# Optimization experiments

Measured on AMD Instinct MI355X. Metric: run time of the kernel, lower is better.

Reference implementation:

```python
import jax, jax.numpy as jnp
import numpy as np

NBATCH, NUP, NDOWN, NMO, NCONF = 8192, 8, 8, 32, 64


def setup_inputs() -> dict:
    key = jax.random.key(0)
    k1, k2, k3, k4 = jax.random.split(key, 4)
    MO = jax.random.normal(k1, (NBATCH, NUP + NDOWN, NMO), dtype=jnp.float32)
    d2MO = jax.random.normal(k2, (NBATCH, NUP + NDOWN, NMO), dtype=jnp.float32)
    # each config = 8 distinct MO column indices per spin (distinct -> invertible A)
    configs_up = jnp.argsort(jax.random.uniform(k3, (NCONF, NMO)), axis=1)[:, :NUP].astype(jnp.int32)
    configs_down = jnp.argsort(jax.random.uniform(k4, (NCONF, NMO)), axis=1)[:, :NDOWN].astype(jnp.int32)
    return {"MO": MO, "d2MO": d2MO, "configs_up": configs_up, "configs_down": configs_down}


def _gather(M, elec_idx, cols):
    # M: (B, nelec, nmo) -> select electron rows then per-config MO columns
    Ms = M[:, elec_idx, :]                  # (B, n, nmo)
    A = jnp.take(Ms, cols, axis=2)          # (B, n, C, n)
    return jnp.transpose(A, (0, 2, 1, 3))   # (B, C, n, n)


def reference(MO, d2MO, configs_up, configs_down):
    nup = configs_up.shape[1]
    ndown = configs_down.shape[1]
    iup = jnp.arange(nup)
    idown = jnp.arange(nup, nup + ndown)

    Aup = _gather(MO, iup, configs_up)       # (B, C, nup, nup)
    Adn = _gather(MO, idown, configs_down)   # (B, C, ndown, ndown)
    d2up = _gather(d2MO, iup, configs_up)
    d2dn = _gather(d2MO, idown, configs_down)

    iAup = jnp.linalg.inv(Aup)
    iAdn = jnp.linalg.inv(Adn)

    # btrace(iA @ d2A) = sum_ij iA[i,j] * d2A[j,i]
    tr = lambda X, Y: jnp.einsum('bcij,bcji->bc', X, Y)
    out = tr(iAup, d2up) + tr(iAdn, d2dn)    # (B, C)

    # return_local_energy=False branch: multiply by product of determinants
    pd = jnp.linalg.det(Aup) * jnp.linalg.det(Adn)
    return -0.5 * out * pd
```

## Files before the change

### kernel.cpp

```cpp
#include <hip/hip_runtime.h>

#define NBATCH 8192
#define NELEC  16
#define NMO    32
#define NCONF  64
#define NS     8
#define TSTR   20
#define TSZ    (NMO * TSTR)

__device__ __forceinline__ void solve8T(const float* __restrict__ MOT,
                                        const float* __restrict__ D2T,
                                        const int (&cols)[NS], int eoff,
                                        float& det_out, float& tr_out)
{
    float A[NS][NS], D[NS][NS];
    #pragma unroll
    for (int j = 0; j < NS; ++j) {
        const float4* pa = (const float4*)(MOT + cols[j] * TSTR + eoff);
        const float4* pd = (const float4*)(D2T + cols[j] * TSTR + eoff);
        float4 a0 = pa[0], a1 = pa[1];
        float4 d0 = pd[0], d1 = pd[1];
        A[j][0] = a0.x; A[j][1] = a0.y; A[j][2] = a0.z; A[j][3] = a0.w;
        A[j][4] = a1.x; A[j][5] = a1.y; A[j][6] = a1.z; A[j][7] = a1.w;
        D[j][0] = d0.x; D[j][1] = d0.y; D[j][2] = d0.z; D[j][3] = d0.w;
        D[j][4] = d1.x; D[j][5] = d1.y; D[j][6] = d1.z; D[j][7] = d1.w;
    }

    float det = 1.0f;
    #pragma unroll
    for (int k = 0; k < NS; ++k) {
        det *= A[k][k];
        float pinv = __builtin_amdgcn_rcpf(A[k][k]);
        A[k][k] = pinv;
        #pragma unroll
        for (int r = k + 1; r < NS; ++r) {
            float m = A[r][k] * pinv;
            #pragma unroll
            for (int c2 = k + 1; c2 < NS; ++c2)
                A[r][c2] = fmaf(-m, A[k][c2], A[r][c2]);
            #pragma unroll
            for (int c2 = 0; c2 < NS; ++c2)
                D[r][c2] = fmaf(-m, D[k][c2], D[r][c2]);
        }
    }

    float tr = 0.0f;
    #pragma unroll
    for (int j = 0; j < NS; ++j) {
        float x[NS];
        #pragma unroll
        for (int i = NS - 1; i >= 0; --i) {
            if (i < j) continue;
            float acc = D[i][j];
            #pragma unroll
            for (int c2 = i + 1; c2 < NS; ++c2)
                acc = fmaf(-A[i][c2], x[c2], acc);
            x[i] = acc * A[i][i];
        }
        tr += x[j];
    }

    det_out = det;
    tr_out  = tr;
}

__global__ __launch_bounds__(256)
void kp_split_kernel(const float* __restrict__ MO,
                     const float* __restrict__ d2MO,
                     const int*   __restrict__ cfg_up,
                     const int*   __restrict__ cfg_dn,
                     float*       __restrict__ out)
{
    __shared__ float smem[2][2][TSZ];

    const int tid  = threadIdx.x;
    const int half = tid >> 7;
    const int u    = tid & 127;
    const int b    = blockIdx.x * 2 + half;

    float* MOT = smem[half][0];
    float* D2T = smem[half][1];

    const float* MOb = MO   + (size_t)b * NELEC * NMO;
    const float* d2b = d2MO + (size_t)b * NELEC * NMO;

    {
        int r = u >> 3;
        int c = (u & 7) * 4;
        float4 v = *(const float4*)(MOb + r * NMO + c);
        float4 w = *(const float4*)(d2b + r * NMO + c);
        MOT[(c + 0) * TSTR + r] = v.x;
        MOT[(c + 1) * TSTR + r] = v.y;
        MOT[(c + 2) * TSTR + r] = v.z;
        MOT[(c + 3) * TSTR + r] = v.w;
        D2T[(c + 0) * TSTR + r] = w.x;
        D2T[(c + 1) * TSTR + r] = w.y;
        D2T[(c + 2) * TSTR + r] = w.z;
        D2T[(c + 3) * TSTR + r] = w.w;
    }
    __syncthreads();

    const int cidx = u >> 1;
    const int s    = u & 1;
    const int* cfg = s ? cfg_dn : cfg_up;
    int4 c0 = ((const int4*)cfg)[cidx * 2 + 0];
    int4 c1 = ((const int4*)cfg)[cidx * 2 + 1];
    const int cols[NS] = {c0.x, c0.y, c0.z, c0.w, c1.x, c1.y, c1.z, c1.w};

    float det, tr;
    solve8T(MOT, D2T, cols, s * NS, det, tr);

    float det_o = __shfl_xor(det, 1);
    float tr_o  = __shfl_xor(tr, 1);
    if (s == 0)
        out[(size_t)b * NCONF + cidx] = -0.5f * (tr + tr_o) * det * det_o;
}

extern "C" void kernel_launch(void* const* d_in, const int* in_sizes, int n_in,
                              void* d_out, int out_size, void* d_ws, size_t ws_size,
                              hipStream_t stream)
{
    const float* MO     = (const float*)d_in[0];
    const float* d2MO   = (const float*)d_in[1];
    const int*   cfg_up = (const int*)d_in[2];
    const int*   cfg_dn = (const int*)d_in[3];
    float* out = (float*)d_out;

    dim3 grid(NBATCH / 2);
    dim3 block(256);
    kp_split_kernel<<<grid, block, 0, stream>>>(MO, d2MO, cfg_up, cfg_dn, out);
}
```

Before: 91.55 us.

## Compute trace via stored LU factors and inverse columns instead of carrying D

Removes the second 8x8 matrix from elimination by storing the L multipliers in A, then builds each column of the inverse by forward and back substitution. Each column is dotted with the matching d2MO row loaded lazily from LDS. This aims to cut register pressure and raise occupancy, at the cost of extra substitution arithmetic per column.

```diff
diff --git a/kernel.cpp b/kernel.cpp
--- a/kernel.cpp
+++ b/kernel.cpp
@@ -13,17 +13,13 @@
                                         const int (&cols)[NS], int eoff,
                                         float& det_out, float& tr_out)
 {
-    float A[NS][NS], D[NS][NS];
+    float A[NS][NS];
     #pragma unroll
     for (int j = 0; j < NS; ++j) {
         const float4* pa = (const float4*)(MOT + cols[j] * TSTR + eoff);
-        const float4* pd = (const float4*)(D2T + cols[j] * TSTR + eoff);
         float4 a0 = pa[0], a1 = pa[1];
-        float4 d0 = pd[0], d1 = pd[1];
         A[j][0] = a0.x; A[j][1] = a0.y; A[j][2] = a0.z; A[j][3] = a0.w;
         A[j][4] = a1.x; A[j][5] = a1.y; A[j][6] = a1.z; A[j][7] = a1.w;
-        D[j][0] = d0.x; D[j][1] = d0.y; D[j][2] = d0.z; D[j][3] = d0.w;
-        D[j][4] = d1.x; D[j][5] = d1.y; D[j][6] = d1.z; D[j][7] = d1.w;
     }
 
     float det = 1.0f;
@@ -35,29 +31,48 @@
         #pragma unroll
         for (int r = k + 1; r < NS; ++r) {
             float m = A[r][k] * pinv;
+            A[r][k] = m;
             #pragma unroll
             for (int c2 = k + 1; c2 < NS; ++c2)
                 A[r][c2] = fmaf(-m, A[k][c2], A[r][c2]);
-            #pragma unroll
-            for (int c2 = 0; c2 < NS; ++c2)
-                D[r][c2] = fmaf(-m, D[k][c2], D[r][c2]);
         }
     }
 
     float tr = 0.0f;
     #pragma unroll
-    for (int j = 0; j < NS; ++j) {
+    for (int k = 0; k < NS; ++k) {
+        const float4* pd = (const float4*)(D2T + cols[k] * TSTR + eoff);
+        float4 d0 = pd[0], d1 = pd[1];
+
+        float y[NS];
+        y[k] = 1.0f;
+        #pragma unroll
+        for (int i = k + 1; i < NS; ++i) {
+            float acc = A[i][k];
+            #pragma unroll
+            for (int j2 = k + 1; j2 < i; ++j2)
+                acc = fmaf(A[i][j2], y[j2], acc);
+            y[i] = -acc;
+        }
+
         float x[NS];
         #pragma unroll
         for (int i = NS - 1; i >= 0; --i) {
-            if (i < j) continue;
-            float acc = D[i][j];
+            float acc = (i >= k) ? y[i] : 0.0f;
             #pragma unroll
             for (int c2 = i + 1; c2 < NS; ++c2)
                 acc = fmaf(-A[i][c2], x[c2], acc);
             x[i] = acc * A[i][i];
         }
-        tr += x[j];
+
+        tr = fmaf(x[0], d0.x, tr);
+        tr = fmaf(x[1], d0.y, tr);
+        tr = fmaf(x[2], d0.z, tr);
+        tr = fmaf(x[3], d0.w, tr);
+        tr = fmaf(x[4], d1.x, tr);
+        tr = fmaf(x[5], d1.y, tr);
+        tr = fmaf(x[6], d1.z, tr);
+        tr = fmaf(x[7], d1.w, tr);
     }
 
     det_out = det;
@@ -65,11 +80,11 @@
 }
 
 __global__ __launch_bounds__(256)
-void kp_split_kernel(const float* __restrict__ MO,
-                     const float* __restrict__ d2MO,
-                     const int*   __restrict__ cfg_up,
-                     const int*   __restrict__ cfg_dn,
-                     float*       __restrict__ out)
+void kp_split2_kernel(const float* __restrict__ MO,
+                      const float* __restrict__ d2MO,
+                      const int*   __restrict__ cfg_up,
+                      const int*   __restrict__ cfg_dn,
+                      float*       __restrict__ out)
 {
     __shared__ float smem[2][2][TSZ];
 
@@ -128,5 +143,5 @@
 
     dim3 grid(NBATCH / 2);
     dim3 block(256);
-    kp_split_kernel<<<grid, block, 0, stream>>>(MO, d2MO, cfg_up, cfg_dn, out);
+    kp_split2_kernel<<<grid, block, 0, stream>>>(MO, d2MO, cfg_up, cfg_dn, out);
 }
```

New measurement: 90.51 us. Within noise of the previous version (-1.1%).

## Compute inverse columns via packed-FMA LU solves and dot with d2 rows

Applied to the files above, without the earlier changes.

Rewrites the per-config 8x8 solve to use packed two-wide FMAs (v2f). It factors A into LU in place and then computes two columns of A^-1 at a time by forward and back substitution. The trace is formed as a dot product with D2 rows loaded from shared memory only when needed, instead of eliminating D alongside A. This drops the D register array, which should lower register pressure and cut scalar FMA count by pairing lanes. In exchange it does extra triangular solves per column pair, and packed-math codegen is not guaranteed.

```diff
diff --git a/kernel.cpp b/kernel.cpp
--- a/kernel.cpp
+++ b/kernel.cpp
@@ -8,56 +8,96 @@
 #define TSTR   20
 #define TSZ    (NMO * TSTR)
 
+typedef float v2f __attribute__((ext_vector_type(2)));
+
+__device__ __forceinline__ v2f pkfma(v2f a, v2f b, v2f c) {
+#if __has_builtin(__builtin_elementwise_fma)
+    return __builtin_elementwise_fma(a, b, c);
+#else
+    return a * b + c;
+#endif
+}
+__device__ __forceinline__ v2f bc2(float s) { return (v2f){s, s}; }
+__device__ __forceinline__ float getel2(const v2f (&R)[4], int j) {
+    return (j & 1) ? R[j >> 1].y : R[j >> 1].x;
+}
+__device__ __forceinline__ void setel2(v2f (&R)[4], int j, float v) {
+    if (j & 1) R[j >> 1].y = v; else R[j >> 1].x = v;
+}
+
 __device__ __forceinline__ void solve8T(const float* __restrict__ MOT,
                                         const float* __restrict__ D2T,
                                         const int (&cols)[NS], int eoff,
                                         float& det_out, float& tr_out)
 {
-    float A[NS][NS], D[NS][NS];
+    v2f A2[NS][4];
     #pragma unroll
     for (int j = 0; j < NS; ++j) {
         const float4* pa = (const float4*)(MOT + cols[j] * TSTR + eoff);
-        const float4* pd = (const float4*)(D2T + cols[j] * TSTR + eoff);
         float4 a0 = pa[0], a1 = pa[1];
-        float4 d0 = pd[0], d1 = pd[1];
-        A[j][0] = a0.x; A[j][1] = a0.y; A[j][2] = a0.z; A[j][3] = a0.w;
-        A[j][4] = a1.x; A[j][5] = a1.y; A[j][6] = a1.z; A[j][7] = a1.w;
-        D[j][0] = d0.x; D[j][1] = d0.y; D[j][2] = d0.z; D[j][3] = d0.w;
-        D[j][4] = d1.x; D[j][5] = d1.y; D[j][6] = d1.z; D[j][7] = d1.w;
+        A2[j][0] = (v2f){a0.x, a0.y};
+        A2[j][1] = (v2f){a0.z, a0.w};
+        A2[j][2] = (v2f){a1.x, a1.y};
+        A2[j][3] = (v2f){a1.z, a1.w};
     }
 
     float det = 1.0f;
     #pragma unroll
     for (int k = 0; k < NS; ++k) {
-        det *= A[k][k];
-        float pinv = __builtin_amdgcn_rcpf(A[k][k]);
-        A[k][k] = pinv;
+        float ukk = getel2(A2[k], k);
+        det *= ukk;
+        float pinv = __builtin_amdgcn_rcpf(ukk);
         #pragma unroll
         for (int r = k + 1; r < NS; ++r) {
-            float m = A[r][k] * pinv;
+            float m = getel2(A2[r], k) * pinv;
+            v2f m2 = bc2(m);
             #pragma unroll
-            for (int c2 = k + 1; c2 < NS; ++c2)
-                A[r][c2] = fmaf(-m, A[k][c2], A[r][c2]);
-            #pragma unroll
-            for (int c2 = 0; c2 < NS; ++c2)
-                D[r][c2] = fmaf(-m, D[k][c2], D[r][c2]);
+            for (int p = (k + 1) >> 1; p < 4; ++p)
+                A2[r][p] = pkfma(-m2, A2[k][p], A2[r][p]);
+            setel2(A2[r], k, m);
         }
+        setel2(A2[k], k, pinv);
     }
 
     float tr = 0.0f;
     #pragma unroll
-    for (int j = 0; j < NS; ++j) {
-        float x[NS];
+    for (int t = 0; t < 4; ++t) {
+        const int k0 = 2 * t, k1 = 2 * t + 1;
+
+        const float4* pd0 = (const float4*)(D2T + cols[k0] * TSTR + eoff);
+        const float4* pd1 = (const float4*)(D2T + cols[k1] * TSTR + eoff);
+        float4 d00 = pd0[0], d01 = pd0[1];
+        float4 d10 = pd1[0], d11 = pd1[1];
+        const float dk0[NS] = {d00.x, d00.y, d00.z, d00.w, d01.x, d01.y, d01.z, d01.w};
+        const float dk1[NS] = {d10.x, d10.y, d10.z, d10.w, d11.x, d11.y, d11.z, d11.w};
+
+        v2f y2[NS];
+        y2[k0] = (v2f){1.0f, 0.0f};
+        y2[k1] = (v2f){-getel2(A2[k1], k0), 1.0f};
+        #pragma unroll
+        for (int i = k1 + 1; i < NS; ++i) {
+            v2f acc = (v2f){0.0f, 0.0f};
+            #pragma unroll
+            for (int j = k0; j < i; ++j)
+                acc = pkfma(bc2(getel2(A2[i], j)), y2[j], acc);
+            y2[i] = -acc;
+        }
+
+        v2f x2[NS];
         #pragma unroll
         for (int i = NS - 1; i >= 0; --i) {
-            if (i < j) continue;
-            float acc = D[i][j];
+            v2f acc = (i >= k0) ? y2[i] : (v2f){0.0f, 0.0f};
             #pragma unroll
             for (int c2 = i + 1; c2 < NS; ++c2)
-                acc = fmaf(-A[i][c2], x[c2], acc);
-            x[i] = acc * A[i][i];
+                acc = pkfma(-bc2(getel2(A2[i], c2)), x2[c2], acc);
+            x2[i] = acc * bc2(getel2(A2[i], i));
         }
-        tr += x[j];
+
+        #pragma unroll
+        for (int i = 0; i < NS; ++i) {
+            tr = fmaf(x2[i].x, dk0[i], tr);
+            tr = fmaf(x2[i].y, dk1[i], tr);
+        }
     }
 
     det_out = det;
@@ -65,11 +105,11 @@
 }
 
 __global__ __launch_bounds__(256)
-void kp_split_kernel(const float* __restrict__ MO,
-                     const float* __restrict__ d2MO,
-                     const int*   __restrict__ cfg_up,
-                     const int*   __restrict__ cfg_dn,
-                     float*       __restrict__ out)
+void kp_pk_kernel(const float* __restrict__ MO,
+                  const float* __restrict__ d2MO,
+                  const int*   __restrict__ cfg_up,
+                  const int*   __restrict__ cfg_dn,
+                  float*       __restrict__ out)
 {
     __shared__ float smem[2][2][TSZ];
 
@@ -128,5 +168,5 @@
 
     dim3 grid(NBATCH / 2);
     dim3 block(256);
-    kp_split_kernel<<<grid, block, 0, stream>>>(MO, d2MO, cfg_up, cfg_dn, out);
+    kp_pk_kernel<<<grid, block, 0, stream>>>(MO, d2MO, cfg_up, cfg_dn, out);
 }
```

New measurement: 89.73 us. 2.0% less time.
